# Kernel optimization log

Hardware: AMD Instinct MI355X
Metric: run time of the kernel (lower is better)

## Reference

```python
import jax, jax.numpy as jnp
import numpy as np

H = 128  # hidden size
I = 19   # input size


def _uniform(key, shape, bound):
    return jax.random.uniform(key, shape, dtype=jnp.float32, minval=-bound, maxval=bound)


def setup_inputs() -> dict:
    key = jax.random.key(0)
    ks = jax.random.split(key, 9)
    bound = 1.0 / np.sqrt(H)  # torch nn.RNN init: U(-1/sqrt(H), 1/sqrt(H))
    x = jax.random.normal(ks[0], (256, 1024, I), dtype=jnp.float32)
    return {
        "x": x,
        "W_ih0": _uniform(ks[1], (H, I), bound),
        "W_hh0": _uniform(ks[2], (H, H), bound),
        "b_ih0": _uniform(ks[3], (H,), bound),
        "b_hh0": _uniform(ks[4], (H,), bound),
        "W_ih1": _uniform(ks[5], (H, H), bound),
        "W_hh1": _uniform(ks[6], (H, H), bound),
        "b_ih1": _uniform(ks[7], (H,), bound),
        "b_hh1": _uniform(ks[8], (H,), bound),
    }


def _rnn_layer(inp, W_ih, W_hh, b_ih, b_hh):
    # inp: [B, T, F]. Precompute input projection for all timesteps (one big GEMM),
    # then scan only the recurrent part: h_t = tanh(pre_t + h_{t-1} @ W_hh^T).
    pre = jnp.einsum('btf,hf->bth', inp, W_ih) + b_ih + b_hh  # [B, T, H]
    h0 = jnp.zeros((inp.shape[0], H), dtype=inp.dtype)

    def step(h, p_t):
        h = jnp.tanh(p_t + h @ W_hh.T)
        return h, h

    _, ys = jax.lax.scan(step, h0, jnp.swapaxes(pre, 0, 1))  # ys: [T, B, H]
    return jnp.swapaxes(ys, 0, 1)  # [B, T, H]


def reference(x, W_ih0, W_hh0, b_ih0, b_hh0, W_ih1, W_hh1, b_ih1, b_hh1):
    out1 = _rnn_layer(x, W_ih0, W_hh0, b_ih0, b_hh0)
    out2 = _rnn_layer(out1, W_ih1, W_hh1, b_ih1, b_hh1)
    return out2
```

## Files before the change

### kernel.cpp

```cpp
#include <hip/hip_runtime.h>
#include <math.h>

#define BATCH 256
#define T 1024
#define IN 19
#define H 128

__device__ __forceinline__ float fast_tanh(float x) {
    float ax = fabsf(x);
    float e  = __expf(2.0f * ax);
    float r  = 1.0f - 2.0f / (e + 1.0f);
    return copysignf(r, x);
}

template <int CTRL>
__device__ __forceinline__ float dppf(float v) {
    return __int_as_float(__builtin_amdgcn_update_dpp(
        0, __float_as_int(v), CTRL, 0xF, 0xF, true));
}
#define XOR1 0xB1
#define XOR2 0x4E
#define XOR8 0x128

__device__ __forceinline__ void sync_fast() {
    asm volatile("s_waitcnt lgkmcnt(0)" ::: "memory");
    __builtin_amdgcn_s_barrier();
    asm volatile("" ::: "memory");
}

__device__ __forceinline__ int uoff(int u) { return (u >> 4) * 20 + (u & 15); }

__global__ __launch_bounds__(512)
__attribute__((amdgpu_waves_per_eu(2, 2)))
void fused_rnn(const float* __restrict__ x,
               const float* __restrict__ Wih0,
               const float* __restrict__ Whh0,
               const float* __restrict__ bih0,
               const float* __restrict__ bhh0,
               const float* __restrict__ Wih1,
               const float* __restrict__ Whh1,
               const float* __restrict__ bih1,
               const float* __restrict__ bhh1,
               float* __restrict__ out) {
    const int b   = blockIdx.x;
    const int tid = threadIdx.x;

    __shared__ __align__(16) float h0ring[4][160];
    __shared__ __align__(16) float h1ring[4][160];
    __shared__ __align__(16) float Bring[4][H];
    __shared__ __align__(16) float projring[4][H];
    __shared__ __align__(16) float xbuf[2][8 * 20];

    if (tid < 128) {
        __builtin_amdgcn_s_setprio(1);
        const bool b0 = tid & 1, b1 = tid & 2, b2 = tid & 8;
        const int s    = (tid & 3) | ((tid & 8) >> 1);
        const int G    = (tid >> 4) * 2 + ((tid >> 2) & 1);
        const int ub   = G * 8;
        const int ufin = ub + (b0 ? 4 : 0) + (b1 ? 2 : 0) + (b2 ? 1 : 0);

        float wA[8][16];
#pragma unroll
        for (int u = 0; u < 8; ++u) {
            const float* wr = Whh0 + (size_t)(ub + u) * H + s * 16;
#pragma unroll
            for (int c = 0; c < 16; c += 4) {
                float4 v = *(const float4*)&wr[c];
                wA[u][c] = v.x; wA[u][c+1] = v.y; wA[u][c+2] = v.z; wA[u][c+3] = v.w;
            }
        }
        {
            const float* wr = Wih0 + ufin * IN;
            const float* xr = x + (size_t)b * T * IN;
            float acc = bih0[ufin] + bhh0[ufin];
#pragma unroll
            for (int f = 0; f < IN; ++f) acc = fmaf(xr[f], wr[f], acc);
            projring[0][ufin] = acc;
        }
        h0ring[3][uoff(ufin)] = 0.0f;
        sync_fast();

        const int so = s * 20;
        const int wo = uoff(ufin);
        for (int ko = 0; ko < T; ko += 8) {
#pragma unroll
            for (int j = 0; j < 8; ++j) {
                const float* hp = &h0ring[(j + 3) & 3][so];
                float pcur = projring[j & 3][ufin];
                float d0=0,d1=0,d2=0,d3=0,d4=0,d5=0,d6=0,d7=0;
#pragma unroll
                for (int c = 0; c < 16; c += 4) {
                    float4 hv = *(const float4*)&hp[c];
                    d0 = fmaf(wA[0][c],hv.x,d0); d0 = fmaf(wA[0][c+1],hv.y,d0); d0 = fmaf(wA[0][c+2],hv.z,d0); d0 = fmaf(wA[0][c+3],hv.w,d0);
                    d1 = fmaf(wA[1][c],hv.x,d1); d1 = fmaf(wA[1][c+1],hv.y,d1); d1 = fmaf(wA[1][c+2],hv.z,d1); d1 = fmaf(wA[1][c+3],hv.w,d1);
                    d2 = fmaf(wA[2][c],hv.x,d2); d2 = fmaf(wA[2][c+1],hv.y,d2); d2 = fmaf(wA[2][c+2],hv.z,d2); d2 = fmaf(wA[2][c+3],hv.w,d2);
                    d3 = fmaf(wA[3][c],hv.x,d3); d3 = fmaf(wA[3][c+1],hv.y,d3); d3 = fmaf(wA[3][c+2],hv.z,d3); d3 = fmaf(wA[3][c+3],hv.w,d3);
                    d4 = fmaf(wA[4][c],hv.x,d4); d4 = fmaf(wA[4][c+1],hv.y,d4); d4 = fmaf(wA[4][c+2],hv.z,d4); d4 = fmaf(wA[4][c+3],hv.w,d4);
                    d5 = fmaf(wA[5][c],hv.x,d5); d5 = fmaf(wA[5][c+1],hv.y,d5); d5 = fmaf(wA[5][c+2],hv.z,d5); d5 = fmaf(wA[5][c+3],hv.w,d5);
                    d6 = fmaf(wA[6][c],hv.x,d6); d6 = fmaf(wA[6][c+1],hv.y,d6); d6 = fmaf(wA[6][c+2],hv.z,d6); d6 = fmaf(wA[6][c+3],hv.w,d6);
                    d7 = fmaf(wA[7][c],hv.x,d7); d7 = fmaf(wA[7][c+1],hv.y,d7); d7 = fmaf(wA[7][c+2],hv.z,d7); d7 = fmaf(wA[7][c+3],hv.w,d7);
                }
                float e0 = (b0 ? d4 : d0) + dppf<XOR1>(b0 ? d0 : d4);
                float e1 = (b0 ? d5 : d1) + dppf<XOR1>(b0 ? d1 : d5);
                float e2 = (b0 ? d6 : d2) + dppf<XOR1>(b0 ? d2 : d6);
                float e3 = (b0 ? d7 : d3) + dppf<XOR1>(b0 ? d3 : d7);
                float g0 = (b1 ? e2 : e0) + dppf<XOR2>(b1 ? e0 : e2);
                float g1 = (b1 ? e3 : e1) + dppf<XOR2>(b1 ? e1 : e3);
                float f  = (b2 ? g1 : g0) + dppf<XOR8>(b2 ? g0 : g1);
                h0ring[j & 3][wo] = fast_tanh(pcur + f);
                sync_fast();
            }
        }
        sync_fast();
        sync_fast();
    } else if (tid < 384) {
        const int p  = tid - 128;
        const bool b0 = p & 1, b1 = p & 2;
        const int s    = (p & 3) | ((p & 8) >> 1);
        const int Gp   = (p >> 4) * 2 + ((p >> 2) & 1);
        const int ub   = Gp * 4;
        const int ufin = ub + (b0 ? 2 : 0) + (b1 ? 1 : 0);

        float wP[4][16];
#pragma unroll
        for (int u = 0; u < 4; ++u) {
            const float* wr = Wih1 + (size_t)(ub + u) * H + s * 16;
#pragma unroll
            for (int c = 0; c < 16; c += 4) {
                float4 v = *(const float4*)&wr[c];
                wP[u][c] = v.x; wP[u][c+1] = v.y; wP[u][c+2] = v.z; wP[u][c+3] = v.w;
            }
        }
        const float biasP = bih1[ufin] + bhh1[ufin];

        const bool hasProj = (p >= 128);
        const int pu = p - 128;
        float wIP[20];
        float biasPr = 0.0f;
        const float* xsrc = x + (size_t)b * T * IN + IN;
        const int idx0  = pu;
        const int idx1  = pu + 128;
        const bool v1   = hasProj && (pu < 24);
        const int slot0 = hasProj ? ((idx0 / IN) * 20 + idx0 % IN) : 0;
        const int slot1 = hasProj ? ((idx1 / IN) * 20 + idx1 % IN) : 0;
        const int XMAX  = (T - 1) * IN - 1;
        float xr0 = 0.0f, xr1 = 0.0f;

        if (hasProj) {
            const float* wr = Wih0 + (size_t)pu * IN;
#pragma unroll
            for (int f = 0; f < IN; ++f) wIP[f] = wr[f];
            wIP[19] = 0.0f;
            biasPr = bih0[pu] + bhh0[pu];
            if (pu < 8) { xbuf[0][pu * 20 + 19] = 0.0f; xbuf[1][pu * 20 + 19] = 0.0f; }
            xbuf[0][slot0] = xsrc[idx0];
            if (v1) xbuf[0][slot1] = xsrc[idx1];
            xr0 = xsrc[152 + idx0];
            if (v1) xr1 = xsrc[152 + idx1];
        }
        sync_fast();

        const int so = s * 20;
        for (int ko = 0; ko < T; ko += 8) {
            const int cb = (ko >> 3) & 1;
#pragma unroll
            for (int j = 0; j < 8; ++j) {
                const float* hp = &h0ring[(j + 3) & 3][so];
                float d0=0,d1=0,d2=0,d3=0;
#pragma unroll
                for (int c = 0; c < 16; c += 4) {
                    float4 hv = *(const float4*)&hp[c];
                    d0 = fmaf(wP[0][c],hv.x,d0); d0 = fmaf(wP[0][c+1],hv.y,d0); d0 = fmaf(wP[0][c+2],hv.z,d0); d0 = fmaf(wP[0][c+3],hv.w,d0);
                    d1 = fmaf(wP[1][c],hv.x,d1); d1 = fmaf(wP[1][c+1],hv.y,d1); d1 = fmaf(wP[1][c+2],hv.z,d1); d1 = fmaf(wP[1][c+3],hv.w,d1);
                    d2 = fmaf(wP[2][c],hv.x,d2); d2 = fmaf(wP[2][c+1],hv.y,d2); d2 = fmaf(wP[2][c+2],hv.z,d2); d2 = fmaf(wP[2][c+3],hv.w,d2);
                    d3 = fmaf(wP[3][c],hv.x,d3); d3 = fmaf(wP[3][c+1],hv.y,d3); d3 = fmaf(wP[3][c+2],hv.z,d3); d3 = fmaf(wP[3][c+3],hv.w,d3);
                }
                float e0 = (b0 ? d2 : d0) + dppf<XOR1>(b0 ? d0 : d2);
                float e1 = (b0 ? d3 : d1) + dppf<XOR1>(b0 ? d1 : d3);
                float g  = (b1 ? e1 : e0) + dppf<XOR2>(b1 ? e0 : e1);
                g += dppf<XOR8>(g);
                if (!(p & 8)) Bring[(j + 3) & 3][ufin] = g + biasP;
                if (hasProj) {
                    const float* xp = &xbuf[cb][j * 20];
                    float4 xv0 = *(const float4*)&xp[0];
                    float4 xv1 = *(const float4*)&xp[4];
                    float4 xv2 = *(const float4*)&xp[8];
                    float4 xv3 = *(const float4*)&xp[12];
                    float4 xv4 = *(const float4*)&xp[16];
                    float p0 = biasPr, p1 = 0.0f;
                    p0 = fmaf(xv0.x, wIP[0],  p0); p1 = fmaf(xv0.y, wIP[1],  p1);
                    p0 = fmaf(xv0.z, wIP[2],  p0); p1 = fmaf(xv0.w, wIP[3],  p1);
                    p0 = fmaf(xv1.x, wIP[4],  p0); p1 = fmaf(xv1.y, wIP[5],  p1);
                    p0 = fmaf(xv1.z, wIP[6],  p0); p1 = fmaf(xv1.w, wIP[7],  p1);
                    p0 = fmaf(xv2.x, wIP[8],  p0); p1 = fmaf(xv2.y, wIP[9],  p1);
                    p0 = fmaf(xv2.z, wIP[10], p0); p1 = fmaf(xv2.w, wIP[11], p1);
                    p0 = fmaf(xv3.x, wIP[12], p0); p1 = fmaf(xv3.y, wIP[13], p1);
                    p0 = fmaf(xv3.z, wIP[14], p0); p1 = fmaf(xv3.w, wIP[15], p1);
                    p0 = fmaf(xv4.x, wIP[16], p0); p1 = fmaf(xv4.y, wIP[17], p1);
                    p0 = fmaf(xv4.z, wIP[18], p0); p1 = fmaf(xv4.w, wIP[19], p1);
                    projring[(j + 1) & 3][pu] = p0 + p1;
                    if (j == 7) {
                        float* xd = xbuf[cb ^ 1];
                        xd[slot0] = xr0;
                        if (v1) xd[slot1] = xr1;
                        const int c2 = (ko >> 3) + 2;
                        int o0 = 152 * c2 + idx0; o0 = o0 > XMAX ? XMAX : o0;
                        int o1 = 152 * c2 + idx1; o1 = o1 > XMAX ? XMAX : o1;
                        xr0 = xsrc[o0];
                        if (v1) xr1 = xsrc[o1];
                    }
                }
                sync_fast();
            }
        }
        {
            const float* hp = &h0ring[3][so];
            float d0=0,d1=0,d2=0,d3=0;
#pragma unroll
            for (int c = 0; c < 16; c += 4) {
                float4 hv = *(const float4*)&hp[c];
                d0 = fmaf(wP[0][c],hv.x,d0); d0 = fmaf(wP[0][c+1],hv.y,d0); d0 = fmaf(wP[0][c+2],hv.z,d0); d0 = fmaf(wP[0][c+3],hv.w,d0);
                d1 = fmaf(wP[1][c],hv.x,d1); d1 = fmaf(wP[1][c+1],hv.y,d1); d1 = fmaf(wP[1][c+2],hv.z,d1); d1 = fmaf(wP[1][c+3],hv.w,d1);
                d2 = fmaf(wP[2][c],hv.x,d2); d2 = fmaf(wP[2][c+1],hv.y,d2); d2 = fmaf(wP[2][c+2],hv.z,d2); d2 = fmaf(wP[2][c+3],hv.w,d2);
                d3 = fmaf(wP[3][c],hv.x,d3); d3 = fmaf(wP[3][c+1],hv.y,d3); d3 = fmaf(wP[3][c+2],hv.z,d3); d3 = fmaf(wP[3][c+3],hv.w,d3);
            }
            float e0 = (b0 ? d2 : d0) + dppf<XOR1>(b0 ? d0 : d2);
            float e1 = (b0 ? d3 : d1) + dppf<XOR1>(b0 ? d1 : d3);
            float g  = (b1 ? e1 : e0) + dppf<XOR2>(b1 ? e0 : e1);
            g += dppf<XOR8>(g);
            if (!(p & 8)) Bring[3][ufin] = g + biasP;
        }
        sync_fast();
        sync_fast();
    } else {
        __builtin_amdgcn_s_setprio(1);
        const int w  = tid - 384;
        const bool b0 = w & 1, b1 = w & 2, b2 = w & 8;
        const int s    = (w & 3) | ((w & 8) >> 1);
        const int G    = (w >> 4) * 2 + ((w >> 2) & 1);
        const int ub   = G * 8;
        const int ufin = ub + (b0 ? 4 : 0) + (b1 ? 2 : 0) + (b2 ? 1 : 0);

        float wA[8][16];
#pragma unroll
        for (int u = 0; u < 8; ++u) {
            const float* wr = Whh1 + (size_t)(ub + u) * H + s * 16;
#pragma unroll
            for (int c = 0; c < 16; c += 4) {
                float4 v = *(const float4*)&wr[c];
                wA[u][c] = v.x; wA[u][c+1] = v.y; wA[u][c+2] = v.z; wA[u][c+3] = v.w;
            }
        }
        float* orow = out + (size_t)b * T * H + ufin;
        float sbuf[8];

        h1ring[3][uoff(ufin)] = 0.0f;
        sync_fast();
        sync_fast();
        sync_fast();

        const int so = s * 20;
        const int wo = uoff(ufin);
        for (int ko = 2; ko < 1026; ko += 8) {
#pragma unroll
            for (int j = 0; j < 8; ++j) {
                const float* hp = &h1ring[(j + 3) & 3][so];
                float Bg = Bring[j & 3][ufin];
                float d0=0,d1=0,d2=0,d3=0,d4=0,d5=0,d6=0,d7=0;
#pragma unroll
                for (int c = 0; c < 16; c += 4) {
                    float4 hv = *(const float4*)&hp[c];
                    d0 = fmaf(wA[0][c],hv.x,d0); d0 = fmaf(wA[0][c+1],hv.y,d0); d0 = fmaf(wA[0][c+2],hv.z,d0); d0 = fmaf(wA[0][c+3],hv.w,d0);
                    d1 = fmaf(wA[1][c],hv.x,d1); d1 = fmaf(wA[1][c+1],hv.y,d1); d1 = fmaf(wA[1][c+2],hv.z,d1); d1 = fmaf(wA[1][c+3],hv.w,d1);
                    d2 = fmaf(wA[2][c],hv.x,d2); d2 = fmaf(wA[2][c+1],hv.y,d2); d2 = fmaf(wA[2][c+2],hv.z,d2); d2 = fmaf(wA[2][c+3],hv.w,d2);
                    d3 = fmaf(wA[3][c],hv.x,d3); d3 = fmaf(wA[3][c+1],hv.y,d3); d3 = fmaf(wA[3][c+2],hv.z,d3); d3 = fmaf(wA[3][c+3],hv.w,d3);
                    d4 = fmaf(wA[4][c],hv.x,d4); d4 = fmaf(wA[4][c+1],hv.y,d4); d4 = fmaf(wA[4][c+2],hv.z,d4); d4 = fmaf(wA[4][c+3],hv.w,d4);
                    d5 = fmaf(wA[5][c],hv.x,d5); d5 = fmaf(wA[5][c+1],hv.y,d5); d5 = fmaf(wA[5][c+2],hv.z,d5); d5 = fmaf(wA[5][c+3],hv.w,d5);
                    d6 = fmaf(wA[6][c],hv.x,d6); d6 = fmaf(wA[6][c+1],hv.y,d6); d6 = fmaf(wA[6][c+2],hv.z,d6); d6 = fmaf(wA[6][c+3],hv.w,d6);
                    d7 = fmaf(wA[7][c],hv.x,d7); d7 = fmaf(wA[7][c+1],hv.y,d7); d7 = fmaf(wA[7][c+2],hv.z,d7); d7 = fmaf(wA[7][c+3],hv.w,d7);
                }
                float e0 = (b0 ? d4 : d0) + dppf<XOR1>(b0 ? d0 : d4);
                float e1 = (b0 ? d5 : d1) + dppf<XOR1>(b0 ? d1 : d5);
                float e2 = (b0 ? d6 : d2) + dppf<XOR1>(b0 ? d2 : d6);
                float e3 = (b0 ? d7 : d3) + dppf<XOR1>(b0 ? d3 : d7);
                float g0 = (b1 ? e2 : e0) + dppf<XOR2>(b1 ? e0 : e2);
                float g1 = (b1 ? e3 : e1) + dppf<XOR2>(b1 ? e1 : e3);
                float f  = (b2 ? g1 : g0) + dppf<XOR8>(b2 ? g0 : g1);
                float h1v = fast_tanh(Bg + f);
                h1ring[j & 3][wo] = h1v;
                sbuf[j] = h1v;
                if (j == 7) {
                    const int t0 = ko - 2;
#pragma unroll
                    for (int i = 0; i < 8; ++i)
                        orow[(size_t)(t0 + i) * H] = sbuf[i];
                }
                sync_fast();
            }
        }
    }
}

extern "C" void kernel_launch(void* const* d_in, const int* in_sizes, int n_in,
                              void* d_out, int out_size, void* d_ws, size_t ws_size,
                              hipStream_t stream) {
    const float* x     = (const float*)d_in[0];
    const float* W_ih0 = (const float*)d_in[1];
    const float* W_hh0 = (const float*)d_in[2];
    const float* b_ih0 = (const float*)d_in[3];
    const float* b_hh0 = (const float*)d_in[4];
    const float* W_ih1 = (const float*)d_in[5];
    const float* W_hh1 = (const float*)d_in[6];
    const float* b_ih1 = (const float*)d_in[7];
    const float* b_hh1 = (const float*)d_in[8];

    float* out = (float*)d_out;

    fused_rnn<<<BATCH, 512, 0, stream>>>(x, W_ih0, W_hh0, b_ih0, b_hh0,
                                         W_ih1, W_hh1, b_ih1, b_hh1, out);
}
```

Baseline: 609.9 us.

## Software-pipeline layer-1 input projection by one extra step in warp-specialized kernel

The middle warp group now loads the layer-0 hidden state into registers in one step and computes the W_ih1 projection in the next, so the LDS read latency is hidden behind a barrier instead of sitting on the critical path. The layer-1 consumer and the layer-0 producer get extra barriers, and the layer-1 schedule shifts by two more steps to match the deeper pipeline. This costs two extra barrier steps of startup latency and keeps more registers live in the projection warps.

```diff
diff --git a/kernel.cpp b/kernel.cpp
--- a/kernel.cpp
+++ b/kernel.cpp
@@ -113,6 +113,8 @@
         }
         sync_fast();
         sync_fast();
+        sync_fast();
+        sync_fast();
     } else if (tid < 384) {
         const int p  = tid - 128;
         const bool b0 = p & 1, b1 = p & 2;
@@ -158,30 +160,67 @@
             xr0 = xsrc[152 + idx0];
             if (v1) xr1 = xsrc[152 + idx1];
         }
-        sync_fast();
+
+        float4 z4 = {0.0f, 0.0f, 0.0f, 0.0f};
+        float4 hb0 = z4, hb1 = z4, hb2 = z4, hb3 = z4;
+
+        sync_fast();
+
+#define P_BCOMP(BSLOT)                                                                \
+        {                                                                             \
+            float d0=0,d1=0,d2=0,d3=0;                                                \
+            d0 = fmaf(wP[0][0],  hb0.x, d0); d0 = fmaf(wP[0][1],  hb0.y, d0);         \
+            d0 = fmaf(wP[0][2],  hb0.z, d0); d0 = fmaf(wP[0][3],  hb0.w, d0);         \
+            d1 = fmaf(wP[1][0],  hb0.x, d1); d1 = fmaf(wP[1][1],  hb0.y, d1);         \
+            d1 = fmaf(wP[1][2],  hb0.z, d1); d1 = fmaf(wP[1][3],  hb0.w, d1);         \
+            d2 = fmaf(wP[2][0],  hb0.x, d2); d2 = fmaf(wP[2][1],  hb0.y, d2);         \
+            d2 = fmaf(wP[2][2],  hb0.z, d2); d2 = fmaf(wP[2][3],  hb0.w, d2);         \
+            d3 = fmaf(wP[3][0],  hb0.x, d3); d3 = fmaf(wP[3][1],  hb0.y, d3);         \
+            d3 = fmaf(wP[3][2],  hb0.z, d3); d3 = fmaf(wP[3][3],  hb0.w, d3);         \
+            d0 = fmaf(wP[0][4],  hb1.x, d0); d0 = fmaf(wP[0][5],  hb1.y, d0);         \
+            d0 = fmaf(wP[0][6],  hb1.z, d0); d0 = fmaf(wP[0][7],  hb1.w, d0);         \
+            d1 = fmaf(wP[1][4],  hb1.x, d1); d1 = fmaf(wP[1][5],  hb1.y, d1);         \
+            d1 = fmaf(wP[1][6],  hb1.z, d1); d1 = fmaf(wP[1][7],  hb1.w, d1);         \
+            d2 = fmaf(wP[2][4],  hb1.x, d2); d2 = fmaf(wP[2][5],  hb1.y, d2);         \
+            d2 = fmaf(wP[2][6],  hb1.z, d2); d2 = fmaf(wP[2][7],  hb1.w, d2);         \
+            d3 = fmaf(wP[3][4],  hb1.x, d3); d3 = fmaf(wP[3][5],  hb1.y, d3);         \
+            d3 = fmaf(wP[3][6],  hb1.z, d3); d3 = fmaf(wP[3][7],  hb1.w, d3);         \
+            d0 = fmaf(wP[0][8],  hb2.x, d0); d0 = fmaf(wP[0][9],  hb2.y, d0);         \
+            d0 = fmaf(wP[0][10], hb2.z, d0); d0 = fmaf(wP[0][11], hb2.w, d0);         \
+            d1 = fmaf(wP[1][8],  hb2.x, d1); d1 = fmaf(wP[1][9],  hb2.y, d1);         \
+            d1 = fmaf(wP[1][10], hb2.z, d1); d1 = fmaf(wP[1][11], hb2.w, d1);         \
+            d2 = fmaf(wP[2][8],  hb2.x, d2); d2 = fmaf(wP[2][9],  hb2.y, d2);         \
+            d2 = fmaf(wP[2][10], hb2.z, d2); d2 = fmaf(wP[2][11], hb2.w, d2);         \
+            d3 = fmaf(wP[3][8],  hb2.x, d3); d3 = fmaf(wP[3][9],  hb2.y, d3);         \
+            d3 = fmaf(wP[3][10], hb2.z, d3); d3 = fmaf(wP[3][11], hb2.w, d3);         \
+            d0 = fmaf(wP[0][12], hb3.x, d0); d0 = fmaf(wP[0][13], hb3.y, d0);         \
+            d0 = fmaf(wP[0][14], hb3.z, d0); d0 = fmaf(wP[0][15], hb3.w, d0);         \
+            d1 = fmaf(wP[1][12], hb3.x, d1); d1 = fmaf(wP[1][13], hb3.y, d1);         \
+            d1 = fmaf(wP[1][14], hb3.z, d1); d1 = fmaf(wP[1][15], hb3.w, d1);         \
+            d2 = fmaf(wP[2][12], hb3.x, d2); d2 = fmaf(wP[2][13], hb3.y, d2);         \
+            d2 = fmaf(wP[2][14], hb3.z, d2); d2 = fmaf(wP[2][15], hb3.w, d2);         \
+            d3 = fmaf(wP[3][12], hb3.x, d3); d3 = fmaf(wP[3][13], hb3.y, d3);         \
+            d3 = fmaf(wP[3][14], hb3.z, d3); d3 = fmaf(wP[3][15], hb3.w, d3);         \
+            float e0 = (b0 ? d2 : d0) + dppf<XOR1>(b0 ? d0 : d2);                     \
+            float e1 = (b0 ? d3 : d1) + dppf<XOR1>(b0 ? d1 : d3);                     \
+            float g  = (b1 ? e1 : e0) + dppf<XOR2>(b1 ? e0 : e1);                     \
+            g += dppf<XOR8>(g);                                                       \
+            if (!(p & 8)) Bring[BSLOT][ufin] = g + biasP;                             \
+        }
 
         const int so = s * 20;
         for (int ko = 0; ko < T; ko += 8) {
             const int cb = (ko >> 3) & 1;
 #pragma unroll
-            for (int j = 0; j < 8; ++j) {
-                const float* hp = &h0ring[(j + 3) & 3][so];
-                float d0=0,d1=0,d2=0,d3=0;
-#pragma unroll
-                for (int c = 0; c < 16; c += 4) {
-                    float4 hv = *(const float4*)&hp[c];
-                    d0 = fmaf(wP[0][c],hv.x,d0); d0 = fmaf(wP[0][c+1],hv.y,d0); d0 = fmaf(wP[0][c+2],hv.z,d0); d0 = fmaf(wP[0][c+3],hv.w,d0);
-                    d1 = fmaf(wP[1][c],hv.x,d1); d1 = fmaf(wP[1][c+1],hv.y,d1); d1 = fmaf(wP[1][c+2],hv.z,d1); d1 = fmaf(wP[1][c+3],hv.w,d1);
-                    d2 = fmaf(wP[2][c],hv.x,d2); d2 = fmaf(wP[2][c+1],hv.y,d2); d2 = fmaf(wP[2][c+2],hv.z,d2); d2 = fmaf(wP[2][c+3],hv.w,d2);
-                    d3 = fmaf(wP[3][c],hv.x,d3); d3 = fmaf(wP[3][c+1],hv.y,d3); d3 = fmaf(wP[3][c+2],hv.z,d3); d3 = fmaf(wP[3][c+3],hv.w,d3);
-                }
-                float e0 = (b0 ? d2 : d0) + dppf<XOR1>(b0 ? d0 : d2);
-                float e1 = (b0 ? d3 : d1) + dppf<XOR1>(b0 ? d1 : d3);
-                float g  = (b1 ? e1 : e0) + dppf<XOR2>(b1 ? e0 : e1);
-                g += dppf<XOR8>(g);
-                if (!(p & 8)) Bring[(j + 3) & 3][ufin] = g + biasP;
+            for (int jj = 0; jj < 8; ++jj) {
+                P_BCOMP(((jj + 2) & 3))
+                {
+                    const float* hp = &h0ring[(jj + 3) & 3][so];
+                    hb0 = *(const float4*)&hp[0];  hb1 = *(const float4*)&hp[4];
+                    hb2 = *(const float4*)&hp[8];  hb3 = *(const float4*)&hp[12];
+                }
                 if (hasProj) {
-                    const float* xp = &xbuf[cb][j * 20];
+                    const float* xp = &xbuf[cb][jj * 20];
                     float4 xv0 = *(const float4*)&xp[0];
                     float4 xv1 = *(const float4*)&xp[4];
                     float4 xv2 = *(const float4*)&xp[8];
@@ -198,8 +237,8 @@
                     p0 = fmaf(xv3.z, wIP[14], p0); p1 = fmaf(xv3.w, wIP[15], p1);
                     p0 = fmaf(xv4.x, wIP[16], p0); p1 = fmaf(xv4.y, wIP[17], p1);
                     p0 = fmaf(xv4.z, wIP[18], p0); p1 = fmaf(xv4.w, wIP[19], p1);
-                    projring[(j + 1) & 3][pu] = p0 + p1;
-                    if (j == 7) {
+                    projring[(jj + 1) & 3][pu] = p0 + p1;
+                    if (jj == 7) {
                         float* xd = xbuf[cb ^ 1];
                         xd[slot0] = xr0;
                         if (v1) xd[slot1] = xr1;
@@ -213,25 +252,18 @@
                 sync_fast();
             }
         }
+        P_BCOMP(2)
         {
             const float* hp = &h0ring[3][so];
-            float d0=0,d1=0,d2=0,d3=0;
-#pragma unroll
-            for (int c = 0; c < 16; c += 4) {
-                float4 hv = *(const float4*)&hp[c];
-                d0 = fmaf(wP[0][c],hv.x,d0); d0 = fmaf(wP[0][c+1],hv.y,d0); d0 = fmaf(wP[0][c+2],hv.z,d0); d0 = fmaf(wP[0][c+3],hv.w,d0);
-                d1 = fmaf(wP[1][c],hv.x,d1); d1 = fmaf(wP[1][c+1],hv.y,d1); d1 = fmaf(wP[1][c+2],hv.z,d1); d1 = fmaf(wP[1][c+3],hv.w,d1);
-                d2 = fmaf(wP[2][c],hv.x,d2); d2 = fmaf(wP[2][c+1],hv.y,d2); d2 = fmaf(wP[2][c+2],hv.z,d2); d2 = fmaf(wP[2][c+3],hv.w,d2);
-                d3 = fmaf(wP[3][c],hv.x,d3); d3 = fmaf(wP[3][c+1],hv.y,d3); d3 = fmaf(wP[3][c+2],hv.z,d3); d3 = fmaf(wP[3][c+3],hv.w,d3);
-            }
-            float e0 = (b0 ? d2 : d0) + dppf<XOR1>(b0 ? d0 : d2);
-            float e1 = (b0 ? d3 : d1) + dppf<XOR1>(b0 ? d1 : d3);
-            float g  = (b1 ? e1 : e0) + dppf<XOR2>(b1 ? e0 : e1);
-            g += dppf<XOR8>(g);
-            if (!(p & 8)) Bring[3][ufin] = g + biasP;
-        }
-        sync_fast();
-        sync_fast();
+            hb0 = *(const float4*)&hp[0];  hb1 = *(const float4*)&hp[4];
+            hb2 = *(const float4*)&hp[8];  hb3 = *(const float4*)&hp[12];
+        }
+        sync_fast();
+        P_BCOMP(3)
+        sync_fast();
+        sync_fast();
+        sync_fast();
+#undef P_BCOMP
     } else {
         __builtin_amdgcn_s_setprio(1);
         const int w  = tid - 384;
@@ -258,10 +290,12 @@
         sync_fast();
         sync_fast();
         sync_fast();
+        sync_fast();
+        sync_fast();
 
         const int so = s * 20;
         const int wo = uoff(ufin);
-        for (int ko = 2; ko < 1026; ko += 8) {
+        for (int ko = 4; ko < 1028; ko += 8) {
 #pragma unroll
             for (int j = 0; j < 8; ++j) {
                 const float* hp = &h1ring[(j + 3) & 3][so];
@@ -290,7 +324,7 @@
                 h1ring[j & 3][wo] = h1v;
                 sbuf[j] = h1v;
                 if (j == 7) {
-                    const int t0 = ko - 2;
+                    const int t0 = ko - 4;
 #pragma unroll
                     for (int i = 0; i < 8; ++i)
                         orow[(size_t)(t0 + i) * H] = sbuf[i];
```

Result: slower. 640.3 us (+5.0%).
